# Kernel optimization log

Hardware: AMD Instinct MI355X
Metric: run time of the kernel (lower is better)

Reference implementation:

```python
import jax, jax.numpy as jnp
import numpy as np

D = 1024
B, S = 4, 2048

def setup_inputs() -> dict:
    key = jax.random.key(0)
    ks = jax.random.split(key, 4)
    scale = 1.0 / np.sqrt(D)
    return {
        "x": jax.random.normal(ks[0], (B, S, D), dtype=jnp.float32),
        "Wq": jax.random.normal(ks[1], (D, D), dtype=jnp.float32) * scale,
        "bq": jnp.zeros((D,), jnp.float32),
        "Wk": jax.random.normal(ks[2], (D, D), dtype=jnp.float32) * scale,
        "bk": jnp.zeros((D,), jnp.float32),
        "Wv": jax.random.normal(ks[3], (D, D), dtype=jnp.float32) * scale,
        "bv": jnp.zeros((D,), jnp.float32),
    }

def reference(x, Wq, bq, Wk, bk, Wv, bv):
    # torch Linear: y = x @ W.T + b
    Q = jnp.einsum('bsd,ed->bse', x, Wq) + bq
    K = jnp.einsum('bsd,ed->bse', x, Wk) + bk
    V = jnp.einsum('bsd,ed->bse', x, Wv) + bv
    # NOTE: original scales by sqrt(K.shape[1]) == sqrt(seq_len), kept faithfully
    dk = K.shape[1]
    logits = jnp.einsum('bqd,bkd->bqk', Q, K) / jnp.sqrt(jnp.asarray(dk, Q.dtype))
    att = jax.nn.softmax(logits, axis=-1)
    return jnp.einsum('bqk,bkd->bqd', att, V)
```

## Files before the change

kernel.cpp:

```cpp
#include <hip/hip_runtime.h>


typedef unsigned short u16;
typedef unsigned int u32;
typedef __bf16 bf16x8 __attribute__((ext_vector_type(8)));
typedef float floatx4 __attribute__((ext_vector_type(4)));

__device__ __forceinline__ u16 f2bf(float f) {
    u32 u = __float_as_uint(f);
    u += 0x7fffu + ((u >> 16) & 1u);
    return (u16)(u >> 16);
}

__device__ __forceinline__ void g2lds16(const void* g, void* l) {
    __builtin_amdgcn_global_load_lds(
        (const __attribute__((address_space(1))) unsigned int*)g,
        (__attribute__((address_space(3))) unsigned int*)l,
        16, 0, 0);
}

__global__ __launch_bounds__(256)
void cvt_all(const float* __restrict__ x, const float* __restrict__ Wq,
             const float* __restrict__ Wk, const float* __restrict__ Wv,
             u16* __restrict__ xb, u16* __restrict__ wall,
             float* __restrict__ rowsum)
{
    const int NX = 2097152;
    const int NW = 262144;
    const int TOT = NX + 3 * NW;
    int i = blockIdx.x * 256 + threadIdx.x;
    if (i >= TOT) {
        int z = i - TOT;
        float4 zz = {0.f, 0.f, 0.f, 0.f};
        ((float4*)rowsum)[z] = zz;
        return;
    }
    const float* src;
    u16* dst;
    int idx;
    if (i < NX) { src = x; dst = xb; idx = i; }
    else {
        int j = i - NX;
        dst = wall; idx = j;
        src = (j < NW) ? Wq : (j < 2 * NW) ? Wk : Wv;
        int jj = (j < NW) ? j : (j < 2 * NW) ? (j - NW) : (j - 2 * NW);
        float4 v = ((const float4*)src)[jj];
        ushort4 o;
        o.x = f2bf(v.x); o.y = f2bf(v.y); o.z = f2bf(v.z); o.w = f2bf(v.w);
        ((ushort4*)dst)[idx] = o;
        return;
    }
    float4 v = ((const float4*)src)[idx];
    ushort4 o;
    o.x = f2bf(v.x); o.y = f2bf(v.y); o.z = f2bf(v.z); o.w = f2bf(v.w);
    ((ushort4*)dst)[idx] = o;
}

template<int MODE>
__global__ __launch_bounds__(256)
void gemm_bt(const u16* __restrict__ A, const u16* __restrict__ B,
             void* __restrict__ Out, const float* __restrict__ bias,
             float scale, int M, int N, int K,
             long long sAz, long long sBz, long long sOz,
             void* __restrict__ Out2, void* __restrict__ Out3,
             const float* __restrict__ bias2, const float* __restrict__ bias3,
             float* __restrict__ rowsum)
{
    __shared__ u16 ldsA[2][128 * 64];
    __shared__ u16 ldsB[2][128 * 64];

    const int tid   = threadIdx.x;
    const int lane  = tid & 63;
    const int wv    = tid >> 6;
    const int wm    = (wv >> 1) * 64;
    const int wn    = (wv & 1) * 64;
    const int lhalf = lane & 15;
    const int quad  = lane >> 4;

    const size_t bz = blockIdx.z;
    A += bz * (size_t)sAz;
    B += bz * (size_t)sBz;

    int tm, tn;
    {
        const int ntn = gridDim.x, ntm = gridDim.y;
        const int lin = blockIdx.y * ntn + blockIdx.x;
        const int GM = 4;
        const int width = GM * ntn;
        const int group = lin / width;
        const int first = group * GM;
        const int gsz   = (ntm - first) < GM ? (ntm - first) : GM;
        const int rem   = lin - group * width;
        tm = first + rem % gsz;
        tn = rem / gsz;
    }
    const int m0 = tm * 128;
    const int n0 = tn * 128;

    const int r8 = lane >> 3;
    const int gc = (lane & 7) ^ r8;
    const u16* pa = A + (size_t)(m0 + wv * 32 + r8) * K + gc * 8;
    const u16* pb = B + (size_t)(n0 + wv * 32 + r8) * K + gc * 8;
    const int lofs = wv * 2048;

    floatx4 zero = {0.f, 0.f, 0.f, 0.f};
    floatx4 acc[4][4];
#pragma unroll
    for (int i = 0; i < 4; ++i)
#pragma unroll
        for (int j = 0; j < 4; ++j) acc[i][j] = zero;

    const int swz = lhalf & 7;

#pragma unroll
    for (int j = 0; j < 4; ++j) {
        g2lds16(pa + (size_t)(j * 8) * K, &ldsA[0][lofs + j * 512]);
        g2lds16(pb + (size_t)(j * 8) * K, &ldsB[0][lofs + j * 512]);
    }
    pa += 64; pb += 64;

    int buf = 0;
    for (int k0 = 0; k0 < K; k0 += 64) {
        __syncthreads();
        if (k0 + 64 < K) {
#pragma unroll
            for (int j = 0; j < 4; ++j) {
                g2lds16(pa + (size_t)(j * 8) * K, &ldsA[buf ^ 1][lofs + j * 512]);
                g2lds16(pb + (size_t)(j * 8) * K, &ldsB[buf ^ 1][lofs + j * 512]);
            }
            pa += 64; pb += 64;
        }

        const u16* lA = ldsA[buf];
        const u16* lB = ldsB[buf];
#pragma unroll
        for (int ks = 0; ks < 2; ++ks) {
            const int c = ks * 4 + quad;
            const int p = c ^ swz;
            bf16x8 af[4], bfv[4];
#pragma unroll
            for (int i = 0; i < 4; ++i)
                af[i] = *(const bf16x8*)(lA + (wm + i * 16 + lhalf) * 64 + p * 8);
#pragma unroll
            for (int j = 0; j < 4; ++j)
                bfv[j] = *(const bf16x8*)(lB + (wn + j * 16 + lhalf) * 64 + p * 8);
#pragma unroll
            for (int i = 0; i < 4; ++i)
#pragma unroll
                for (int j = 0; j < 4; ++j)
                    acc[i][j] = __builtin_amdgcn_mfma_f32_16x16x32_bf16(
                        af[i], bfv[j], acc[i][j], 0, 0, 0);
        }
        buf ^= 1;
    }

#pragma unroll
    for (int i = 0; i < 4; ++i) {
        const int mb = m0 + wm + i * 16 + quad * 4;
        if (MODE == 3) {
#pragma unroll
            for (int j = 0; j < 4; ++j) {
                const int n = n0 + wn + j * 16 + lhalf;
                if (n < 1024) {
                    const float bb = bias[n];
#pragma unroll
                    for (int r = 0; r < 4; ++r)
                        ((u16*)Out)[(size_t)(mb + r) * 1024 + n] =
                            f2bf(acc[i][j][r] + bb);
                } else if (n < 2048) {
                    const float bb = bias2[n - 1024];
#pragma unroll
                    for (int r = 0; r < 4; ++r)
                        ((u16*)Out2)[(size_t)(mb + r) * 1024 + (n - 1024)] =
                            f2bf(acc[i][j][r] + bb);
                } else {
                    const int d = n - 2048;
                    const float bb = bias3[d];
                    const int b = mb >> 11;
                    const int s0 = mb & 2047;
                    ushort4 w;
                    w.x = f2bf(acc[i][j][0] + bb);
                    w.y = f2bf(acc[i][j][1] + bb);
                    w.z = f2bf(acc[i][j][2] + bb);
                    w.w = f2bf(acc[i][j][3] + bb);
                    *(ushort4*)((u16*)Out3 + (size_t)b * 2097152 +
                                (size_t)d * 2048 + s0) = w;
                }
            }
        } else if (MODE == 4) {
#pragma unroll
            for (int r = 0; r < 4; ++r) {
                const int m = mb + r;
                float rs = 0.f;
#pragma unroll
                for (int j = 0; j < 4; ++j) {
                    const int n = n0 + wn + j * 16 + lhalf;
                    const float e = __expf(acc[i][j][r] * scale);
                    ((u16*)Out)[bz * (size_t)sOz + (size_t)m * N + n] = f2bf(e);
                    rs += e;
                }
                rs += __shfl_xor(rs, 1, 64);
                rs += __shfl_xor(rs, 2, 64);
                rs += __shfl_xor(rs, 4, 64);
                rs += __shfl_xor(rs, 8, 64);
                if (lhalf == 0)
                    atomicAdd(&rowsum[bz * 2048 + m], rs);
            }
        } else {
            float4 rs4 = *(const float4*)&rowsum[bz * 2048 + mb];
            float rinv[4];
            rinv[0] = __builtin_amdgcn_rcpf(rs4.x);
            rinv[1] = __builtin_amdgcn_rcpf(rs4.y);
            rinv[2] = __builtin_amdgcn_rcpf(rs4.z);
            rinv[3] = __builtin_amdgcn_rcpf(rs4.w);
#pragma unroll
            for (int j = 0; j < 4; ++j) {
                const int n = n0 + wn + j * 16 + lhalf;
#pragma unroll
                for (int r = 0; r < 4; ++r)
                    ((float*)Out)[bz * (size_t)sOz + (size_t)(mb + r) * N + n] =
                        acc[i][j][r] * rinv[r];
            }
        }
    }
}

extern "C" void kernel_launch(void* const* d_in, const int* in_sizes, int n_in,
                              void* d_out, int out_size, void* d_ws, size_t ws_size,
                              hipStream_t stream)
{
    const float* x  = (const float*)d_in[0];
    const float* Wq = (const float*)d_in[1];
    const float* bq = (const float*)d_in[2];
    const float* Wk = (const float*)d_in[3];
    const float* bk = (const float*)d_in[4];
    const float* Wv = (const float*)d_in[5];
    const float* bv = (const float*)d_in[6];
    float* out = (float*)d_out;

    const int B = 4, S = 2048, D = 1024;
    const long long SD = (long long)S * D;
    const long long SS = (long long)S * S;
    const long long BSD = (long long)B * SD;
    const long long DD = (long long)D * D;

    u16* xb   = (u16*)d_ws;
    u16* wall = xb   + BSD;
    u16* Qb   = wall + 3 * DD;
    u16* Kb   = Qb   + BSD;
    u16* Vt   = Kb   + BSD;
    u16* Sc   = Vt   + BSD;
    float* rowsum = (float*)(Sc + B * SS);

    cvt_all<<<dim3(11272), 256, 0, stream>>>(x, Wq, Wk, Wv, xb, wall, rowsum);

    gemm_bt<3><<<dim3(3 * D / 128, (B * S) / 128, 1), 256, 0, stream>>>(
        xb, wall, Qb, bq, 1.f, B * S, 3 * D, D, 0, 0, 0,
        Kb, Vt, bk, bv, nullptr);

    const float sc = 0.022097086912079608f;
    gemm_bt<4><<<dim3(S / 128, S / 128, B), 256, 0, stream>>>(
        Qb, Kb, Sc, nullptr, sc, S, S, D, SD, SD, SS,
        nullptr, nullptr, nullptr, nullptr, rowsum);

    gemm_bt<5><<<dim3(D / 128, S / 128, B), 256, 0, stream>>>(
        Sc, Vt, out, nullptr, 1.f, S, D, S, SS, SD, SD,
        nullptr, nullptr, nullptr, nullptr, rowsum);
}
```

Measured before the change: 251.9 us.

## Load B operand directly from global into registers, staging only A in LDS

The GEMM no longer stages the B tile through shared memory. Each wave loads its own B fragments straight from global memory into registers, double-buffered across a loop unrolled by two k-steps, while A still goes through LDS with async global-to-LDS loads. This halves LDS usage and removes the LDS reads for B, which may allow higher occupancy. The cost is more register pressure and global loads that are less coalesced, since lanes fetch 16-byte chunks from scattered rows. B data is also loaded redundantly, because the two waves sharing a column half each fetch it.

```diff
diff --git a/kernel.cpp b/kernel.cpp
--- a/kernel.cpp
+++ b/kernel.cpp
@@ -67,7 +67,6 @@
              float* __restrict__ rowsum)
 {
     __shared__ u16 ldsA[2][128 * 64];
-    __shared__ u16 ldsB[2][128 * 64];
 
     const int tid   = threadIdx.x;
     const int lane  = tid & 63;
@@ -100,8 +99,9 @@
     const int r8 = lane >> 3;
     const int gc = (lane & 7) ^ r8;
     const u16* pa = A + (size_t)(m0 + wv * 32 + r8) * K + gc * 8;
-    const u16* pb = B + (size_t)(n0 + wv * 32 + r8) * K + gc * 8;
     const int lofs = wv * 2048;
+
+    const u16* pbq = B + (size_t)(n0 + wn + lhalf) * K + quad * 8;
 
     floatx4 zero = {0.f, 0.f, 0.f, 0.f};
     floatx4 acc[4][4];
@@ -112,46 +112,80 @@
 
     const int swz = lhalf & 7;
 
-#pragma unroll
-    for (int j = 0; j < 4; ++j) {
+    bf16x8 b0[2][4], b1[2][4];
+
+#pragma unroll
+    for (int j = 0; j < 4; ++j)
         g2lds16(pa + (size_t)(j * 8) * K, &ldsA[0][lofs + j * 512]);
-        g2lds16(pb + (size_t)(j * 8) * K, &ldsB[0][lofs + j * 512]);
-    }
-    pa += 64; pb += 64;
-
-    int buf = 0;
-    for (int k0 = 0; k0 < K; k0 += 64) {
+    pa += 64;
+#pragma unroll
+    for (int ks = 0; ks < 2; ++ks)
+#pragma unroll
+        for (int j = 0; j < 4; ++j)
+            b0[ks][j] = *(const bf16x8*)(pbq + (size_t)(j * 16) * K + ks * 32);
+
+    for (int k0 = 0; k0 < K; k0 += 128) {
         __syncthreads();
-        if (k0 + 64 < K) {
-#pragma unroll
-            for (int j = 0; j < 4; ++j) {
-                g2lds16(pa + (size_t)(j * 8) * K, &ldsA[buf ^ 1][lofs + j * 512]);
-                g2lds16(pb + (size_t)(j * 8) * K, &ldsB[buf ^ 1][lofs + j * 512]);
-            }
-            pa += 64; pb += 64;
-        }
-
-        const u16* lA = ldsA[buf];
-        const u16* lB = ldsB[buf];
-#pragma unroll
-        for (int ks = 0; ks < 2; ++ks) {
-            const int c = ks * 4 + quad;
-            const int p = c ^ swz;
-            bf16x8 af[4], bfv[4];
-#pragma unroll
-            for (int i = 0; i < 4; ++i)
-                af[i] = *(const bf16x8*)(lA + (wm + i * 16 + lhalf) * 64 + p * 8);
+        {
 #pragma unroll
             for (int j = 0; j < 4; ++j)
-                bfv[j] = *(const bf16x8*)(lB + (wn + j * 16 + lhalf) * 64 + p * 8);
-#pragma unroll
-            for (int i = 0; i < 4; ++i)
+                g2lds16(pa + (size_t)(j * 8) * K, &ldsA[1][lofs + j * 512]);
+            pa += 64;
+            const u16* pk = pbq + (k0 + 64);
+#pragma unroll
+            for (int ks = 0; ks < 2; ++ks)
 #pragma unroll
                 for (int j = 0; j < 4; ++j)
-                    acc[i][j] = __builtin_amdgcn_mfma_f32_16x16x32_bf16(
-                        af[i], bfv[j], acc[i][j], 0, 0, 0);
-        }
-        buf ^= 1;
+                    b1[ks][j] = *(const bf16x8*)(pk + (size_t)(j * 16) * K + ks * 32);
+        }
+        {
+            const u16* lA = ldsA[0];
+#pragma unroll
+            for (int ks = 0; ks < 2; ++ks) {
+                const int p = (ks * 4 + quad) ^ swz;
+                bf16x8 af[4];
+#pragma unroll
+                for (int i = 0; i < 4; ++i)
+                    af[i] = *(const bf16x8*)(lA + (wm + i * 16 + lhalf) * 64 + p * 8);
+#pragma unroll
+                for (int i = 0; i < 4; ++i)
+#pragma unroll
+                    for (int j = 0; j < 4; ++j)
+                        acc[i][j] = __builtin_amdgcn_mfma_f32_16x16x32_bf16(
+                            af[i], b0[ks][j], acc[i][j], 0, 0, 0);
+            }
+        }
+
+        __syncthreads();
+        if (k0 + 128 < K) {
+#pragma unroll
+            for (int j = 0; j < 4; ++j)
+                g2lds16(pa + (size_t)(j * 8) * K, &ldsA[0][lofs + j * 512]);
+            pa += 64;
+            const u16* pk = pbq + (k0 + 128);
+#pragma unroll
+            for (int ks = 0; ks < 2; ++ks)
+#pragma unroll
+                for (int j = 0; j < 4; ++j)
+                    b0[ks][j] = *(const bf16x8*)(pk + (size_t)(j * 16) * K + ks * 32);
+        }
+        {
+            const u16* lA = ldsA[1];
+#pragma unroll
+            for (int ks = 0; ks < 2; ++ks) {
+                const int p = (ks * 4 + quad) ^ swz;
+                bf16x8 af[4];
+#pragma unroll
+                for (int i = 0; i < 4; ++i)
+                    af[i] = *(const bf16x8*)(lA + (wm + i * 16 + lhalf) * 64 + p * 8);
+#pragma unroll
+                for (int i = 0; i < 4; ++i)
+#pragma unroll
+                    for (int j = 0; j < 4; ++j)
+                        acc[i][j] = __builtin_amdgcn_mfma_f32_16x16x32_bf16(
+                            af[i], b1[ks][j], acc[i][j], 0, 0, 0);
+            }
+        }
     }
 
 #pragma unroll
```

New measurement: 374.4 us. +48.6%, slower.
